# Kernel tuning notes

Hardware: AMD Instinct MI355X
Metric: run time of the kernel (lower is better)

Reference implementation:

```python
import jax, jax.numpy as jnp
import numpy as np

B, DIM, FMAP = 32, 256, 32
HEADS, DK, DV = 8, 32, 64
N = FMAP * FMAP
SCALE = DK ** -0.5
EPS = 1e-5


def _bn(x, g, b):
    # training-mode BatchNorm2d: biased batch stats over (B, H, W)
    m = x.mean(axis=(0, 2, 3), keepdims=True)
    v = x.var(axis=(0, 2, 3), keepdims=True)
    return (x - m) * jax.lax.rsqrt(v + EPS) * g[None, :, None, None] + b[None, :, None, None]


def _conv1x1(x, W):
    # 1x1 conv, no bias: [O,C] x [B,C,H,W] -> [B,O,H,W]
    return jnp.einsum('oc,bchw->bohw', W, x)


def _make_pos_indices():
    r = np.arange(FMAP)
    pos = np.stack(np.meshgrid(r, r, indexing='ij'), axis=-1).reshape(-1, 2)  # [N,2]
    rel = np.abs(pos[:, None, :] - pos[None, :, :])  # [N,N,2]
    return (rel[..., 0] * FMAP + rel[..., 1]).astype(np.int32)


def setup_inputs() -> dict:
    key = jax.random.key(0)
    ks = jax.random.split(key, 16)
    s = 0.02
    return {
        'x': jax.random.normal(ks[0], (B, DIM, FMAP, FMAP), jnp.float32),
        'Wq': jax.random.normal(ks[1], (HEADS * DK, DIM), jnp.float32) * s,
        'gamma_q': jax.random.uniform(ks[2], (HEADS * DK,), jnp.float32, 0.5, 1.5),
        'beta_q': jax.random.normal(ks[3], (HEADS * DK,), jnp.float32) * 0.1,
        'Wk': jax.random.normal(ks[4], (HEADS * DK, DIM), jnp.float32) * s,
        'gamma_k': jax.random.uniform(ks[5], (HEADS * DK,), jnp.float32, 0.5, 1.5),
        'beta_k': jax.random.normal(ks[6], (HEADS * DK,), jnp.float32) * 0.1,
        'Wv': jax.random.normal(ks[7], (HEADS * DV, DIM), jnp.float32) * s,
        'gamma_v': jax.random.uniform(ks[8], (HEADS * DV,), jnp.float32, 0.5, 1.5),
        'beta_v': jax.random.normal(ks[9], (HEADS * DV,), jnp.float32) * 0.1,
        'Wo': jax.random.normal(ks[10], (DIM, HEADS * DV), jnp.float32) * s,
        'b_o': jax.random.normal(ks[11], (DIM,), jnp.float32) * 0.1,
        'gamma_o': jax.random.uniform(ks[12], (DIM,), jnp.float32, 0.5, 1.5),
        'beta_o': jax.random.normal(ks[13], (DIM,), jnp.float32) * 0.1,
        'pos_table': jax.random.normal(ks[14], (N, HEADS), jnp.float32) * 0.02,
        'pos_indices': jnp.asarray(_make_pos_indices()),
    }


def reference(x, Wq, gamma_q, beta_q, Wk, gamma_k, beta_k, Wv, gamma_v, beta_v,
              Wo, b_o, gamma_o, beta_o, pos_table, pos_indices):
    b = x.shape[0]
    q = _bn(_conv1x1(x, Wq), gamma_q, beta_q)
    k = _bn(_conv1x1(x, Wk), gamma_k, beta_k)
    v = _bn(_conv1x1(x, Wv), gamma_v, beta_v)

    def to_heads(t):
        bb, c, H, W = t.shape  # b (h d) H W -> b h (H W) d
        return t.reshape(bb, HEADS, c // HEADS, H * W).transpose(0, 1, 3, 2)

    q, k, v = to_heads(q), to_heads(k), to_heads(v)
    dots = jnp.einsum('bhid,bhjd->bhij', q, k) * SCALE  # [b,h,N,N]
    bias = pos_table[pos_indices]                        # gather -> [N,N,h]
    dots = dots + jnp.transpose(bias, (2, 0, 1))[None] / SCALE
    attn = jax.nn.softmax(dots, axis=-1)
    out = jnp.einsum('bhij,bhjd->bhid', attn, v)         # [b,h,N,dv]
    out = out.transpose(0, 1, 3, 2).reshape(b, HEADS * DV, FMAP, FMAP)
    out = jax.nn.gelu(out, approximate=False)
    out = _conv1x1(out, Wo) + b_o[None, :, None, None]
    return _bn(out, gamma_o, beta_o)
```

## Files before the change

kernel.cpp:

```cpp
#include <hip/hip_runtime.h>
#include <stdint.h>


typedef unsigned int uint;
typedef unsigned short ushort;

typedef __bf16 bf16x8 __attribute__((ext_vector_type(8)));
typedef short  shortx4 __attribute__((ext_vector_type(4)));
typedef float  floatx4 __attribute__((ext_vector_type(4)));

__device__ __forceinline__ float bf2f(ushort u){ uint t = ((uint)u)<<16; float f; __builtin_memcpy(&f,&t,4); return f; }
__device__ __forceinline__ ushort f2bf(float f){ uint u; __builtin_memcpy(&u,&f,4); return (ushort)((u + 0x7fffu + ((u>>16)&1u))>>16); }
__device__ __forceinline__ uint pack2(float a, float b){ return (uint)f2bf(a) | ((uint)f2bf(b)<<16); }
__device__ __forceinline__ uint fbits(float f){ uint u; __builtin_memcpy(&u,&f,4); return u; }
__device__ __forceinline__ float asf(uint u){ float f; __builtin_memcpy(&f,&u,4); return f; }
__device__ __forceinline__ uint4 cvt8(const float* p){
  float4 a = *(const float4*)p; float4 b = *(const float4*)(p+4);
  uint4 r; r.x = pack2(a.x,a.y); r.y = pack2(a.z,a.w); r.z = pack2(b.x,b.y); r.w = pack2(b.z,b.w);
  return r;
}

__device__ __forceinline__ floatx4 mfma32(bf16x8 a, bf16x8 b, floatx4 c){
  return __builtin_amdgcn_mfma_f32_16x16x32_bf16(a,b,c,0,0,0);
}
__device__ __forceinline__ floatx4 mfma16(shortx4 a, shortx4 b, floatx4 c){
  return __builtin_amdgcn_mfma_f32_16x16x16bf16_1k(a,b,c,0,0,0);
}

#define OFF_KB   16777216u
#define OFF_VT   33554432u
#define OFF_BIAS 67108864u
#define OFF_XT   83886080u
#define OFF_WBF  100663296u
#define OFF_SQK  101187584u
#define OFF_GT   83886080u
#define OFF_SUM  117440512u
#define OFF_OSUM 117448704u
#define OFF_AB   117450752u
#define WS_NEED  117460992u

__global__ __launch_bounds__(256) void k_prep(const float* __restrict__ x,
    const float* __restrict__ Wq, const float* __restrict__ Wk, const float* __restrict__ Wv,
    const float* __restrict__ pt,
    ushort* __restrict__ xT, ushort* __restrict__ wbf, ushort* __restrict__ bias){
  __shared__ ushort tr[64*66];
  int bid = blockIdx.x;
  int tid = threadIdx.x;
  if (bid < 256){
    int idx = (bid*256 + tid)*4;
    const float* src; int off;
    if (idx < 65536){ src = Wq; off = idx; }
    else if (idx < 131072){ src = Wk; off = idx - 65536; }
    else { src = Wv; off = idx - 131072; }
    float4 f = *(const float4*)(src + off);
    uint2 o; o.x = pack2(f.x,f.y); o.y = pack2(f.z,f.w);
    *(uint2*)(wbf + idx) = o;
  } else if (bid < 2304){
    int b2 = bid - 256;
    int cb = (b2 & 3)*64;
    int nb = ((b2>>2)&15)*64;
    int b  = b2>>6;
    int cl = tid>>2, n0 = (tid&3)*16;
    const float* src = x + (((size_t)b*256 + cb + cl)<<10) + nb + n0;
    ushort u16[16];
    #pragma unroll
    for(int q4=0;q4<4;q4++){
      float4 f = *(const float4*)(src + q4*4);
      u16[q4*4+0]=f2bf(f.x); u16[q4*4+1]=f2bf(f.y); u16[q4*4+2]=f2bf(f.z); u16[q4*4+3]=f2bf(f.w);
    }
    #pragma unroll
    for(int j=0;j<16;j++) tr[(n0+j)*66 + cl] = u16[j];
    __syncthreads();
    int nl = tid>>2, c0 = (tid&3)*16;
    uint o2[8];
    #pragma unroll
    for(int k=0;k<8;k++) o2[k] = *(const uint*)&tr[nl*66 + c0 + k*2];
    ushort* dst = xT + (((size_t)b*1024 + nb + nl)<<8) + cb + c0;
    *(uint4*)dst     = *(uint4*)&o2[0];
    *(uint4*)(dst+8) = *(uint4*)&o2[4];
  } else {
    int t = (bid-2304)*256 + tid;
    int lane = t & 63;
    int jsub = (t>>6)&63;
    int isub = (t>>12)&63;
    int h = t>>18;
    int i  = isub*16 + (lane&15);
    int jb = jsub*16 + ((lane>>4)<<2);
    int r1 = i>>5, c1 = i&31;
    const float BS = 1.44269504088896f*5.65685424949238f;
    ushort o[4];
    #pragma unroll
    for(int r=0;r<4;r++){
      int j = jb + r;
      int dr = r1 - (j>>5); dr = dr<0 ? -dr : dr;
      int dc = c1 - (j&31); dc = dc<0 ? -dc : dc;
      o[r] = f2bf(pt[(dr*32+dc)*8 + h] * BS);
    }
    uint2 ow; ow.x = (uint)o[0] | ((uint)o[1]<<16); ow.y = (uint)o[2] | ((uint)o[3]<<16);
    ((uint2*)bias)[t] = ow;
  }
}

__global__ __launch_bounds__(256) void k_qkv(const ushort* __restrict__ xT,
    const ushort* __restrict__ wbf,
    ushort* __restrict__ qb, ushort* __restrict__ kb, ushort* __restrict__ vt,
    float2* __restrict__ sqk){
  __shared__ ushort smem[18432];
  ushort* Ax = smem;
  ushort* Aw = smem + 9216;
  int bid = blockIdx.x;
  int nt = bid & 7; int ot = (bid>>3)&7; int b = bid>>6;
  int nb = nt*128, ob = ot*128;
  int mode = (ob < 256) ? 0 : (ob < 512 ? 1 : 2);
  int t = threadIdx.x, w = t>>6, l = t&63;
  int wr = w>>1, wc = w&1;
  int sr = t>>1, sc = (t&1)*32;
  const ushort* xrow = xT + (((size_t)b*1024 + nb + sr)<<8) + sc;
  const ushort* wrow = wbf + (size_t)(ob + sr)*256 + sc;
  floatx4 acc[4][4];
  #pragma unroll
  for(int m=0;m<4;m++)
    #pragma unroll
    for(int nf=0;nf<4;nf++) acc[m][nf] = (floatx4){0.f,0.f,0.f,0.f};

  for(int kc=0;kc<4;kc++){
    #pragma unroll
    for(int q4=0;q4<4;q4++){
      *(uint4*)&Ax[sr*72 + sc + q4*8] = *(const uint4*)(xrow + kc*64 + q4*8);
      *(uint4*)&Aw[sr*72 + sc + q4*8] = *(const uint4*)(wrow + kc*64 + q4*8);
    }
    __syncthreads();
    const ushort* Abuf = (mode==2)? Aw : Ax;
    const ushort* Bbuf = (mode==2)? Ax : Aw;
    int arb = (mode==2)? wc*64 : wr*64;
    int brb = (mode==2)? wr*64 : wc*64;
    #pragma unroll
    for(int kk=0;kk<2;kk++){
      bf16x8 af[4], bfr[4];
      #pragma unroll
      for(int m=0;m<4;m++)  af[m]  = *(const bf16x8*)&Abuf[(arb + m*16 + (l&15))*72 + kk*32 + (l>>4)*8];
      #pragma unroll
      for(int nf=0;nf<4;nf++) bfr[nf] = *(const bf16x8*)&Bbuf[(brb + nf*16 + (l&15))*72 + kk*32 + (l>>4)*8];
      #pragma unroll
      for(int m=0;m<4;m++)
        #pragma unroll
        for(int nf=0;nf<4;nf++)
          acc[m][nf] = mfma32(af[m], bfr[nf], acc[m][nf]);
    }
    __syncthreads();
  }

  int contrib = (nt*32 + b)*2 + wr;
  if (mode < 2){
    #pragma unroll
    for(int nf=0;nf<4;nf++){
      int o = ob + wc*64 + nf*16 + (l&15);
      float s1=0.f, s2=0.f;
      #pragma unroll
      for(int m=0;m<4;m++){
        #pragma unroll
        for(int r=0;r<4;r++){
          float val = acc[m][nf][r];
          s1 += val; s2 += val*val;
        }
      }
      s1 += __shfl_xor(s1,16,64); s1 += __shfl_xor(s1,32,64);
      s2 += __shfl_xor(s2,16,64); s2 += __shfl_xor(s2,32,64);
      if (l < 16){
        float2 p; p.x = s1; p.y = s2;
        sqk[(size_t)o*512 + contrib] = p;
      }
    }
  } else {
    #pragma unroll
    for(int m=0;m<4;m++){
      #pragma unroll
      for(int r=0;r<4;r++){
        int o  = ob + wc*64 + m*16 + (l>>4)*4 + r;
        float s1=0.f, s2=0.f;
        #pragma unroll
        for(int nf=0;nf<4;nf++){
          float val = acc[m][nf][r];
          s1 += val; s2 += val*val;
        }
        s1 += __shfl_xor(s1,1,64); s1 += __shfl_xor(s1,2,64); s1 += __shfl_xor(s1,4,64); s1 += __shfl_xor(s1,8,64);
        s2 += __shfl_xor(s2,1,64); s2 += __shfl_xor(s2,2,64); s2 += __shfl_xor(s2,4,64); s2 += __shfl_xor(s2,8,64);
        if ((l&15)==0){
          float2 p; p.x = s1; p.y = s2;
          sqk[(size_t)o*512 + contrib] = p;
        }
      }
    }
  }

  ushort* ep = smem + w*4608;
  if (mode < 2){
    #pragma unroll
    for(int m=0;m<4;m++)
      #pragma unroll
      for(int nf=0;nf<4;nf++){
        int lo = nf*16 + (l&15);
        #pragma unroll
        for(int r=0;r<4;r++){
          int ln = m*16 + (l>>4)*4 + r;
          ep[ln*72 + lo] = f2bf(acc[m][nf][r]);
        }
      }
    ushort* outb = (mode==0)? qb : kb;
    #pragma unroll
    for(int p=0;p<8;p++){
      int rr = p*8 + (l>>3);
      int ci = (l&7)*8;
      uint4 v = *(const uint4*)&ep[rr*72 + ci];
      int n = nb + wr*64 + rr;
      int o = ob + wc*64 + ci;
      int oc = o & 255;
      int h = oc>>5, d = oc&31;
      *(uint4*)(outb + (((size_t)(b*8+h)<<10) + n)*32 + d) = v;
    }
  } else {
    #pragma unroll
    for(int m=0;m<4;m++)
      #pragma unroll
      for(int nf=0;nf<4;nf++){
        int ln = nf*16 + (l&15);
        #pragma unroll
        for(int r=0;r<4;r++){
          int lo = m*16 + (l>>4)*4 + r;
          ep[lo*72 + ln] = f2bf(acc[m][nf][r]);
        }
      }
    #pragma unroll
    for(int p=0;p<8;p++){
      int rr = p*8 + (l>>3);
      int ci = (l&7)*8;
      uint4 v = *(const uint4*)&ep[rr*72 + ci];
      int o  = ob + wc*64 + rr;
      int ov = o - 512;
      int h = ov>>6, dv = ov&63;
      int n = nb + wr*64 + ci;
      *(uint4*)(vt + ((((size_t)b*8 + h)*64 + dv)<<10) + n) = v;
    }
  }
}

__global__ __launch_bounds__(256) void k_coef(const float2* __restrict__ sqk,
    const float* gq, const float* bq, const float* gk, const float* bk,
    const float* gvp, const float* bvp, float* __restrict__ ab){
  __shared__ float red[4][2];
  int ch = blockIdx.x;
  int t = threadIdx.x, w = t>>6, l = t&63;
  float2 v0 = sqk[(size_t)ch*512 + t];
  float2 v1 = sqk[(size_t)ch*512 + 256 + t];
  float s1 = v0.x + v1.x, s2 = v0.y + v1.y;
  s1 += __shfl_xor(s1,1,64); s2 += __shfl_xor(s2,1,64);
  s1 += __shfl_xor(s1,2,64); s2 += __shfl_xor(s2,2,64);
  s1 += __shfl_xor(s1,4,64); s2 += __shfl_xor(s2,4,64);
  s1 += __shfl_xor(s1,8,64); s2 += __shfl_xor(s2,8,64);
  s1 += __shfl_xor(s1,16,64); s2 += __shfl_xor(s2,16,64);
  s1 += __shfl_xor(s1,32,64); s2 += __shfl_xor(s2,32,64);
  if (l==0){ red[w][0]=s1; red[w][1]=s2; }
  __syncthreads();
  if (t==0){
    float S1 = red[0][0]+red[1][0]+red[2][0]+red[3][0];
    float S2 = red[0][1]+red[1][1]+red[2][1]+red[3][1];
    float mean = S1 * (1.0f/32768.0f);
    float var  = S2 * (1.0f/32768.0f) - mean*mean;
    float inv  = rsqrtf(var + 1e-5f);
    float g, be, ex;
    if (ch < 256){ g = gq[ch]; be = bq[ch]; ex = 1.44269504088896f*0.17677669529664f; }
    else if (ch < 512){ g = gk[ch-256]; be = bk[ch-256]; ex = 1.0f; }
    else { g = gvp[ch-512]; be = bvp[ch-512]; ex = 1.0f; }
    ab[ch*2]   = g*inv*ex;
    ab[ch*2+1] = (be - mean*g*inv)*ex;
  }
}

__device__ __forceinline__ bf16x8 qprep(uint4 raw, const float* __restrict__ abq,
                                        const float* __restrict__ abk){
  uint w4[4] = {raw.x, raw.y, raw.z, raw.w};
  ushort o[8];
  #pragma unroll
  for(int p=0;p<4;p++){
    float lo = asf(w4[p]<<16), hi = asf(w4[p] & 0xffff0000u);
    float q0 = abq[p*4+0]*lo + abq[p*4+1];
    float q1 = abq[p*4+2]*hi + abq[p*4+3];
    o[p*2]   = f2bf(q0 * abk[p*4+0]);
    o[p*2+1] = f2bf(q1 * abk[p*4+2]);
  }
  bf16x8 r; __builtin_memcpy(&r, o, 16);
  return r;
}

__global__ __launch_bounds__(256) void k_attn(const ushort* __restrict__ qb, const ushort* __restrict__ kb,
    const ushort* __restrict__ vt, const ushort* __restrict__ bias,
    const float* __restrict__ ab, ushort* __restrict__ GT){
  __shared__ ushort smem[9216];
  ushort* kt  = smem;
  ushort* vtl = smem + 2560;
  ushort* gbuf = smem;
  int bid = blockIdx.x;
  int h = bid & 7;
  int itile = (bid>>3)&7;
  int b = bid>>6;
  int t = threadIdx.x, w = t>>6, l = t&63;
  int isub0 = itile*8 + w*2;
  size_t bh = (size_t)b*8 + h;

  const float* abq = ab + (size_t)(h*32 + (l>>4)*8)*2;
  const float* abk = ab + (size_t)(256 + h*32 + (l>>4)*8)*2;
  uint4 qr0 = *(const uint4*)(qb + ((bh<<10) + isub0*16 + (l&15))*32 + (l>>4)*8);
  uint4 qr1 = *(const uint4*)(qb + ((bh<<10) + (isub0+1)*16 + (l&15))*32 + (l>>4)*8);
  bf16x8 qf0 = qprep(qr0, abq, abk);
  bf16x8 qf1 = qprep(qr1, abq, abk);

  const shortx4 vones = { (short)0x3F80, (short)0x3F80, (short)0x3F80, (short)0x3F80 };
  floatx4 lf0 = {0.f,0.f,0.f,0.f}, lf1 = {0.f,0.f,0.f,0.f};
  floatx4 O0[4] = {{0.f,0.f,0.f,0.f},{0.f,0.f,0.f,0.f},{0.f,0.f,0.f,0.f},{0.f,0.f,0.f,0.f}};
  floatx4 O1[4] = {{0.f,0.f,0.f,0.f},{0.f,0.f,0.f,0.f},{0.f,0.f,0.f,0.f},{0.f,0.f,0.f,0.f}};
  int sr = t>>2, scq = t&3;
  const uint2* bp0 = (const uint2*)bias + (((size_t)h*64 + isub0)*64)*64 + l;
  const uint2* bp1 = bp0 + 64*64;

  for(int jt=0;jt<16;jt++){
    int jbase = jt*64;
    *(uint4*)&kt[sr*40 + scq*8] = *(const uint4*)(kb + ((bh<<10) + jbase + sr)*32 + scq*8);
    const ushort* vsrc = vt + ((bh*64 + sr)<<10) + jbase + scq*16;
    *(uint4*)&vtl[sr*72 + scq*16]     = *(const uint4*)vsrc;
    *(uint4*)&vtl[sr*72 + scq*16 + 8] = *(const uint4*)(vsrc + 8);
    __syncthreads();

    __builtin_amdgcn_s_setprio(1);
    #pragma unroll
    for(int js=0;js<4;js++){
      uint2 bw0 = bp0[js*64];
      uint2 bw1 = bp1[js*64];
      bf16x8 kf = *(const bf16x8*)&kt[(js*16 + (l&15))*40 + (l>>4)*8];
      floatx4 c0 = { asf(bw0.x<<16), asf(bw0.x & 0xffff0000u), asf(bw0.y<<16), asf(bw0.y & 0xffff0000u) };
      floatx4 c1 = { asf(bw1.x<<16), asf(bw1.x & 0xffff0000u), asf(bw1.y<<16), asf(bw1.y & 0xffff0000u) };
      floatx4 S0 = mfma32(kf, qf0, c0);
      floatx4 S1 = mfma32(kf, qf1, c1);
      float a0 = __builtin_amdgcn_exp2f(S0[0]);
      float a1 = __builtin_amdgcn_exp2f(S0[1]);
      float a2 = __builtin_amdgcn_exp2f(S0[2]);
      float a3 = __builtin_amdgcn_exp2f(S0[3]);
      float b0 = __builtin_amdgcn_exp2f(S1[0]);
      float b1 = __builtin_amdgcn_exp2f(S1[1]);
      float b2 = __builtin_amdgcn_exp2f(S1[2]);
      float b3 = __builtin_amdgcn_exp2f(S1[3]);
      uint2 pu0, pu1;
      pu0.x = __builtin_amdgcn_perm(fbits(a1), fbits(a0), 0x07060302u);
      pu0.y = __builtin_amdgcn_perm(fbits(a3), fbits(a2), 0x07060302u);
      pu1.x = __builtin_amdgcn_perm(fbits(b1), fbits(b0), 0x07060302u);
      pu1.y = __builtin_amdgcn_perm(fbits(b3), fbits(b2), 0x07060302u);
      shortx4 p0, p1;
      __builtin_memcpy(&p0, &pu0, 8);
      __builtin_memcpy(&p1, &pu1, 8);
      lf0 = mfma16(vones, p0, lf0);
      lf1 = mfma16(vones, p1, lf1);
      #pragma unroll
      for(int d=0;d<4;d++){
        shortx4 vf = *(const shortx4*)&vtl[(d*16 + (l&15))*72 + js*16 + (l>>4)*4];
        O0[d] = mfma16(vf, p0, O0[d]);
        O1[d] = mfma16(vf, p1, O1[d]);
      }
    }
    __builtin_amdgcn_s_setprio(0);
    bp0 += 256; bp1 += 256;
    __syncthreads();
  }

  float invl0 = 1.0f/lf0[0];
  float invl1 = 1.0f/lf1[0];

  #pragma unroll
  for(int ii=0;ii<2;ii++){
    float invl = ii ? invl1 : invl0;
    #pragma unroll
    for(int d=0;d<4;d++){
      floatx4 Ov = ii ? O1[d] : O0[d];
      const float* abv = ab + (size_t)(512 + h*64 + d*16 + (l>>4)*4)*2;
      float4 e01 = *(const float4*)abv;
      float4 e23 = *(const float4*)(abv + 4);
      float av[4] = {e01.x, e01.z, e23.x, e23.z};
      float bv[4] = {e01.y, e01.w, e23.y, e23.w};
      ushort gu[4];
      #pragma unroll
      for(int r=0;r<4;r++){
        float o = av[r]*(Ov[r]*invl) + bv[r];
        float g = 0.5f*o*(1.0f + erff(o*0.70710678118655f));
        gu[r] = f2bf(g);
      }
      uint2 gw; gw.x = (uint)gu[0] | ((uint)gu[1]<<16); gw.y = (uint)gu[2] | ((uint)gu[3]<<16);
      *(uint2*)&gbuf[w*2304 + (ii*16 + (l&15))*72 + d*16 + (l>>4)*4] = gw;
    }
  }
  __syncthreads();
  int ibase = itile*128 + w*32;
  #pragma unroll
  for(int p8=0;p8<4;p8++){
    int rl = (l>>3) + p8*8;
    int ck = l&7;
    uint4 g4 = *(uint4*)&gbuf[w*2304 + rl*72 + ck*8];
    int n = ibase + rl;
    *(uint4*)(GT + ((size_t)(b*1024 + n))*512 + h*64 + ck*8) = g4;
  }
}

__global__ __launch_bounds__(256) void k_oconv(const ushort* __restrict__ GT, const float* __restrict__ Wo,
    const float* __restrict__ bo, ushort* __restrict__ opre, float2* __restrict__ soc){
  __shared__ ushort smem[18432];
  ushort* Aw = smem;
  ushort* Ag = smem + 9216;
  int bid = blockIdx.x;
  int nt = bid & 15; int ot = (bid>>4)&3; int b = bid>>6;
  int nb = nt*64, ob = ot*64;
  int t = threadIdx.x, w = t>>6, l = t&63;
  int sr = t>>2, sc = (t&3)*16;
  const float*  wsrc = Wo + (size_t)(ob + sr)*512 + sc;
  const ushort* gsrc = GT + ((size_t)b*1024 + nb + sr)*512 + sc;
  floatx4 acc[4] = {{0.f,0.f,0.f,0.f},{0.f,0.f,0.f,0.f},{0.f,0.f,0.f,0.f},{0.f,0.f,0.f,0.f}};
  for(int kc=0;kc<8;kc++){
    *(uint4*)&Aw[sr*72+sc]   = cvt8(wsrc + kc*64);
    *(uint4*)&Aw[sr*72+sc+8] = cvt8(wsrc + kc*64 + 8);
    *(uint4*)&Ag[sr*72+sc]   = *(const uint4*)(gsrc + kc*64);
    *(uint4*)&Ag[sr*72+sc+8] = *(const uint4*)(gsrc + kc*64 + 8);
    __syncthreads();
    #pragma unroll
    for(int kk=0;kk<2;kk++){
      bf16x8 af = *(const bf16x8*)&Aw[(w*16 + (l&15))*72 + kk*32 + (l>>4)*8];
      #pragma unroll
      for(int ns=0;ns<4;ns++){
        bf16x8 bfv = *(const bf16x8*)&Ag[(ns*16 + (l&15))*72 + kk*32 + (l>>4)*8];
        acc[ns] = mfma32(af, bfv, acc[ns]);
      }
    }
    __syncthreads();
  }
  ushort* ep = smem + w*1152;
  int contrib = nt*32 + b;
  #pragma unroll
  for(int r_=0;r_<4;r_++){
    int oloc = w*16 + (l>>4)*4 + r_;
    int o = ob + oloc;
    float bias_o = bo[o];
    float s1=0.f, s2=0.f;
    #pragma unroll
    for(int ns=0;ns<4;ns++){
      float val = acc[ns][r_] + bias_o;
      ep[((l>>4)*4 + r_)*72 + ns*16 + (l&15)] = f2bf(val);
      s1 += val; s2 += val*val;
    }
    s1 += __shfl_xor(s1,1,64); s1 += __shfl_xor(s1,2,64); s1 += __shfl_xor(s1,4,64); s1 += __shfl_xor(s1,8,64);
    s2 += __shfl_xor(s2,1,64); s2 += __shfl_xor(s2,2,64); s2 += __shfl_xor(s2,4,64); s2 += __shfl_xor(s2,8,64);
    if ((l&15)==0){
      float2 p; p.x = s1; p.y = s2;
      soc[(size_t)o*512 + contrib] = p;
    }
  }
  {
    int rr = l>>2, cseg = (l&3)*16;
    uint4 v0 = *(const uint4*)&ep[rr*72 + cseg];
    uint4 v1 = *(const uint4*)&ep[rr*72 + cseg + 8];
    int o = ob + w*16 + rr;
    ushort* dst = opre + (((size_t)(b*256+o))<<10) + nb + cseg;
    *(uint4*)dst     = v0;
    *(uint4*)(dst+8) = v1;
  }
}

__global__ __launch_bounds__(256) void k_ocoef(const float2* __restrict__ soc,
    const float* __restrict__ go, const float* __restrict__ beo, float* __restrict__ oc){
  __shared__ float red[4][2];
  int ch = blockIdx.x;
  int t = threadIdx.x, w = t>>6, l = t&63;
  float2 v0 = soc[(size_t)ch*512 + t];
  float2 v1 = soc[(size_t)ch*512 + 256 + t];
  float s1 = v0.x + v1.x, s2 = v0.y + v1.y;
  s1 += __shfl_xor(s1,1,64); s2 += __shfl_xor(s2,1,64);
  s1 += __shfl_xor(s1,2,64); s2 += __shfl_xor(s2,2,64);
  s1 += __shfl_xor(s1,4,64); s2 += __shfl_xor(s2,4,64);
  s1 += __shfl_xor(s1,8,64); s2 += __shfl_xor(s2,8,64);
  s1 += __shfl_xor(s1,16,64); s2 += __shfl_xor(s2,16,64);
  s1 += __shfl_xor(s1,32,64); s2 += __shfl_xor(s2,32,64);
  if (l==0){ red[w][0]=s1; red[w][1]=s2; }
  __syncthreads();
  if (t==0){
    float S1 = red[0][0]+red[1][0]+red[2][0]+red[3][0];
    float S2 = red[0][1]+red[1][1]+red[2][1]+red[3][1];
    float mean = S1 * (1.0f/32768.0f);
    float var  = S2 * (1.0f/32768.0f) - mean*mean;
    float inv  = rsqrtf(var + 1e-5f);
    float a = go[ch]*inv;
    oc[ch*2]   = a;
    oc[ch*2+1] = beo[ch] - mean*a;
  }
}

__global__ __launch_bounds__(256) void k_bnout(const ushort* __restrict__ opre, const float* __restrict__ oc,
    float* __restrict__ out){
  size_t e = ((size_t)blockIdx.x*256 + threadIdx.x)*4;
  int o = (int)((e>>10)&255);
  float a = oc[o*2], bb = oc[o*2+1];
  uint2 raw = *(const uint2*)(opre + e);
  float4 ov;
  ov.x = a*asf(raw.x<<16)           + bb;
  ov.y = a*asf(raw.x & 0xffff0000u) + bb;
  ov.z = a*asf(raw.y<<16)           + bb;
  ov.w = a*asf(raw.y & 0xffff0000u) + bb;
  *(float4*)(out + e) = ov;
}

extern "C" void kernel_launch(void* const* d_in, const int* in_sizes, int n_in,
                              void* d_out, int out_size, void* d_ws, size_t ws_size,
                              hipStream_t stream){
  (void)in_sizes; (void)n_in; (void)out_size;
  const float* x   = (const float*)d_in[0];
  const float* Wq  = (const float*)d_in[1];
  const float* gq  = (const float*)d_in[2];
  const float* bq  = (const float*)d_in[3];
  const float* Wk  = (const float*)d_in[4];
  const float* gk  = (const float*)d_in[5];
  const float* bk  = (const float*)d_in[6];
  const float* Wv  = (const float*)d_in[7];
  const float* gvp = (const float*)d_in[8];
  const float* bvp = (const float*)d_in[9];
  const float* Wo  = (const float*)d_in[10];
  const float* bo  = (const float*)d_in[11];
  const float* go  = (const float*)d_in[12];
  const float* beo = (const float*)d_in[13];
  const float* pt  = (const float*)d_in[14];

  char* ws = (char*)d_ws;
  if (ws_size < (size_t)WS_NEED) return;
  ushort* qb   = (ushort*)(ws);
  ushort* kb   = (ushort*)(ws + OFF_KB);
  ushort* vt   = (ushort*)(ws + OFF_VT);
  ushort* bias = (ushort*)(ws + OFF_BIAS);
  ushort* xT   = (ushort*)(ws + OFF_XT);
  ushort* wbf  = (ushort*)(ws + OFF_WBF);
  ushort* GT   = (ushort*)(ws + OFF_GT);
  ushort* opre = (ushort*)(ws);
  float2* sqk  = (float2*)(ws + OFF_SQK);
  float2* soc  = (float2*)(ws + OFF_KB);
  float* oc    = (float*)(ws + OFF_OSUM);
  float* ab    = (float*)(ws + OFF_AB);

  k_prep<<<10496,256,0,stream>>>(x, Wq, Wk, Wv, pt, xT, wbf, bias);
  k_qkv<<<2048,256,0,stream>>>(xT, wbf, qb, kb, vt, sqk);
  k_coef<<<1024,256,0,stream>>>(sqk, gq, bq, gk, bk, gvp, bvp, ab);
  k_attn<<<2048,256,0,stream>>>(qb, kb, vt, bias, ab, GT);
  k_oconv<<<2048,256,0,stream>>>(GT, Wo, bo, opre, soc);
  k_ocoef<<<256,256,0,stream>>>(soc, go, beo, oc);
  k_bnout<<<8192,256,0,stream>>>(opre, oc, (float*)d_out);
}
```

Before: 307.3 us.

## Fuse x transpose and bf16 conversion into QKV GEMM tile loading

Drops the separate pass in the prep kernel that converted x to bf16 and transposed it into a workspace buffer. The QKV GEMM now reads fp32 x directly, packs channel pairs to bf16 and stores them transposed into an XOR-swizzled shared-memory tile, which removes a full write and re-read of the transposed activations. The cost is that x is re-read and re-converted by each of the 8 output-channel tiles, and the shared-memory writes are scattered. It also removes the s_setprio hints from the attention inner loop.

```diff
diff --git a/kernel.cpp b/kernel.cpp
--- a/kernel.cpp
+++ b/kernel.cpp
@@ -30,7 +30,6 @@
 #define OFF_KB   16777216u
 #define OFF_VT   33554432u
 #define OFF_BIAS 67108864u
-#define OFF_XT   83886080u
 #define OFF_WBF  100663296u
 #define OFF_SQK  101187584u
 #define OFF_GT   83886080u
@@ -39,11 +38,10 @@
 #define OFF_AB   117450752u
 #define WS_NEED  117460992u
 
-__global__ __launch_bounds__(256) void k_prep(const float* __restrict__ x,
+__global__ __launch_bounds__(256) void k_prep(
     const float* __restrict__ Wq, const float* __restrict__ Wk, const float* __restrict__ Wv,
     const float* __restrict__ pt,
-    ushort* __restrict__ xT, ushort* __restrict__ wbf, ushort* __restrict__ bias){
-  __shared__ ushort tr[64*66];
+    ushort* __restrict__ wbf, ushort* __restrict__ bias){
   int bid = blockIdx.x;
   int tid = threadIdx.x;
   if (bid < 256){
@@ -55,31 +53,8 @@
     float4 f = *(const float4*)(src + off);
     uint2 o; o.x = pack2(f.x,f.y); o.y = pack2(f.z,f.w);
     *(uint2*)(wbf + idx) = o;
-  } else if (bid < 2304){
-    int b2 = bid - 256;
-    int cb = (b2 & 3)*64;
-    int nb = ((b2>>2)&15)*64;
-    int b  = b2>>6;
-    int cl = tid>>2, n0 = (tid&3)*16;
-    const float* src = x + (((size_t)b*256 + cb + cl)<<10) + nb + n0;
-    ushort u16[16];
-    #pragma unroll
-    for(int q4=0;q4<4;q4++){
-      float4 f = *(const float4*)(src + q4*4);
-      u16[q4*4+0]=f2bf(f.x); u16[q4*4+1]=f2bf(f.y); u16[q4*4+2]=f2bf(f.z); u16[q4*4+3]=f2bf(f.w);
-    }
-    #pragma unroll
-    for(int j=0;j<16;j++) tr[(n0+j)*66 + cl] = u16[j];
-    __syncthreads();
-    int nl = tid>>2, c0 = (tid&3)*16;
-    uint o2[8];
-    #pragma unroll
-    for(int k=0;k<8;k++) o2[k] = *(const uint*)&tr[nl*66 + c0 + k*2];
-    ushort* dst = xT + (((size_t)b*1024 + nb + nl)<<8) + cb + c0;
-    *(uint4*)dst     = *(uint4*)&o2[0];
-    *(uint4*)(dst+8) = *(uint4*)&o2[4];
   } else {
-    int t = (bid-2304)*256 + tid;
+    int t = (bid-256)*256 + tid;
     int lane = t & 63;
     int jsub = (t>>6)&63;
     int isub = (t>>12)&63;
@@ -101,7 +76,7 @@
   }
 }
 
-__global__ __launch_bounds__(256) void k_qkv(const ushort* __restrict__ xT,
+__global__ __launch_bounds__(256) void k_qkv(const float* __restrict__ x,
     const ushort* __restrict__ wbf,
     ushort* __restrict__ qb, ushort* __restrict__ kb, ushort* __restrict__ vt,
     float2* __restrict__ sqk){
@@ -115,8 +90,12 @@
   int t = threadIdx.x, w = t>>6, l = t&63;
   int wr = w>>1, wc = w&1;
   int sr = t>>1, sc = (t&1)*32;
-  const ushort* xrow = xT + (((size_t)b*1024 + nb + sr)<<8) + sc;
   const ushort* wrow = wbf + (size_t)(ob + sr)*256 + sc;
+  int cp = t>>3;
+  int ngx = (t&7)*16;
+  int gsw = (((cp>>2) ^ (t&7))<<3) + ((cp&3)<<1);
+  const float* xbase = x + (((size_t)b*256 + cp*2)<<10) + nb + ngx;
+
   floatx4 acc[4][4];
   #pragma unroll
   for(int m=0;m<4;m++)
@@ -126,26 +105,49 @@
   for(int kc=0;kc<4;kc++){
     #pragma unroll
     for(int q4=0;q4<4;q4++){
-      *(uint4*)&Ax[sr*72 + sc + q4*8] = *(const uint4*)(xrow + kc*64 + q4*8);
       *(uint4*)&Aw[sr*72 + sc + q4*8] = *(const uint4*)(wrow + kc*64 + q4*8);
     }
+    const float* xr = xbase + ((size_t)kc<<16);
+    #pragma unroll
+    for(int hh=0;hh<2;hh++){
+      float r0[8], r1[8];
+      *(float4*)&r0[0] = *(const float4*)(xr + hh*8);
+      *(float4*)&r0[4] = *(const float4*)(xr + hh*8 + 4);
+      *(float4*)&r1[0] = *(const float4*)(xr + 1024 + hh*8);
+      *(float4*)&r1[4] = *(const float4*)(xr + 1024 + hh*8 + 4);
+      #pragma unroll
+      for(int j=0;j<8;j++){
+        *(uint*)&Ax[(ngx + hh*8 + j)*72 + gsw] = pack2(r0[j], r1[j]);
+      }
+    }
     __syncthreads();
-    const ushort* Abuf = (mode==2)? Aw : Ax;
-    const ushort* Bbuf = (mode==2)? Ax : Aw;
-    int arb = (mode==2)? wc*64 : wr*64;
-    int brb = (mode==2)? wr*64 : wc*64;
+    int gl = l>>4;
+    int xrb = wr*64, wrb = wc*64;
     #pragma unroll
     for(int kk=0;kk<2;kk++){
-      bf16x8 af[4], bfr[4];
-      #pragma unroll
-      for(int m=0;m<4;m++)  af[m]  = *(const bf16x8*)&Abuf[(arb + m*16 + (l&15))*72 + kk*32 + (l>>4)*8];
-      #pragma unroll
-      for(int nf=0;nf<4;nf++) bfr[nf] = *(const bf16x8*)&Bbuf[(brb + nf*16 + (l&15))*72 + kk*32 + (l>>4)*8];
-      #pragma unroll
-      for(int m=0;m<4;m++)
+      bf16x8 xf[4], wf[4];
+      #pragma unroll
+      for(int m=0;m<4;m++){
+        int srow = (4*wr + m) & 7;
+        int g2 = ((kk*4 + gl) ^ srow) << 3;
+        xf[m] = *(const bf16x8*)&Ax[(xrb + m*16 + (l&15))*72 + g2];
+      }
+      #pragma unroll
+      for(int nf=0;nf<4;nf++)
+        wf[nf] = *(const bf16x8*)&Aw[(wrb + nf*16 + (l&15))*72 + kk*32 + gl*8];
+      if (mode < 2){
         #pragma unroll
-        for(int nf=0;nf<4;nf++)
-          acc[m][nf] = mfma32(af[m], bfr[nf], acc[m][nf]);
+        for(int m=0;m<4;m++)
+          #pragma unroll
+          for(int nf=0;nf<4;nf++)
+            acc[m][nf] = mfma32(xf[m], wf[nf], acc[m][nf]);
+      } else {
+        #pragma unroll
+        for(int m=0;m<4;m++)
+          #pragma unroll
+          for(int nf=0;nf<4;nf++)
+            acc[m][nf] = mfma32(wf[m], xf[nf], acc[m][nf]);
+      }
     }
     __syncthreads();
   }
@@ -330,7 +332,6 @@
     *(uint4*)&vtl[sr*72 + scq*16 + 8] = *(const uint4*)(vsrc + 8);
     __syncthreads();
 
-    __builtin_amdgcn_s_setprio(1);
     #pragma unroll
     for(int js=0;js<4;js++){
       uint2 bw0 = bp0[js*64];
@@ -365,7 +366,6 @@
         O1[d] = mfma16(vf, p1, O1[d]);
       }
     }
-    __builtin_amdgcn_s_setprio(0);
     bp0 += 256; bp1 += 256;
     __syncthreads();
   }
@@ -441,8 +441,7 @@
   int contrib = nt*32 + b;
   #pragma unroll
   for(int r_=0;r_<4;r_++){
-    int oloc = w*16 + (l>>4)*4 + r_;
-    int o = ob + oloc;
+    int o = ob + w*16 + (l>>4)*4 + r_;
     float bias_o = bo[o];
     float s1=0.f, s2=0.f;
     #pragma unroll
@@ -537,7 +536,6 @@
   ushort* kb   = (ushort*)(ws + OFF_KB);
   ushort* vt   = (ushort*)(ws + OFF_VT);
   ushort* bias = (ushort*)(ws + OFF_BIAS);
-  ushort* xT   = (ushort*)(ws + OFF_XT);
   ushort* wbf  = (ushort*)(ws + OFF_WBF);
   ushort* GT   = (ushort*)(ws + OFF_GT);
   ushort* opre = (ushort*)(ws);
@@ -546,8 +544,8 @@
   float* oc    = (float*)(ws + OFF_OSUM);
   float* ab    = (float*)(ws + OFF_AB);
 
-  k_prep<<<10496,256,0,stream>>>(x, Wq, Wk, Wv, pt, xT, wbf, bias);
-  k_qkv<<<2048,256,0,stream>>>(xT, wbf, qb, kb, vt, sqk);
+  k_prep<<<8448,256,0,stream>>>(Wq, Wk, Wv, pt, wbf, bias);
+  k_qkv<<<2048,256,0,stream>>>(x, wbf, qb, kb, vt, sqk);
   k_coef<<<1024,256,0,stream>>>(sqk, gq, bq, gk, bk, gvp, bvp, ab);
   k_attn<<<2048,256,0,stream>>>(qb, kb, vt, bias, ab, GT);
   k_oconv<<<2048,256,0,stream>>>(GT, Wo, bo, opre, soc);
```

Measured after the change: 326.0 us. 6.1% more time.
